# Kernel optimization log

Hardware: AMD Instinct MI355X
Metric: run time of the kernel (lower is better)

## Reference

```python
import jax, jax.numpy as jnp
import numpy as np

HEADS = 8
HEAD_DIM = 64
SCALE = HEAD_DIM ** -0.5


def setup_inputs() -> dict:
    key = jax.random.key(0)
    ks = jax.random.split(key, 5)
    d_model, inner = 1024, HEADS * HEAD_DIM  # 512
    x = jax.random.normal(ks[0], (2, 2048, d_model), dtype=jnp.float32)
    # torch Linear weights stored pre-transposed as [in, out]
    Wq = jax.random.normal(ks[1], (d_model, inner), dtype=jnp.float32) * (d_model ** -0.5)
    Wkv = jax.random.normal(ks[2], (d_model, 2 * inner), dtype=jnp.float32) * (d_model ** -0.5)
    Wo = jax.random.normal(ks[3], (inner, d_model), dtype=jnp.float32) * (inner ** -0.5)
    bo = jnp.zeros((d_model,), dtype=jnp.float32)
    return {"x": x, "Wq": Wq, "Wkv": Wkv, "Wo": Wo, "bo": bo}


def reference(x, Wq, Wkv, Wo, bo):
    b, n, _ = x.shape
    q = x @ Wq                       # [b, n, h*d]
    kv = x @ Wkv                     # [b, n, 2*h*d] (self-attention: context = x)
    k, v = jnp.split(kv, 2, axis=-1)

    def split_heads(t):
        return t.reshape(b, n, HEADS, HEAD_DIM).transpose(0, 2, 1, 3)  # [b, h, n, d]

    q, k, v = map(split_heads, (q, k, v))
    sim = jnp.einsum('bhid,bhjd->bhij', q, k) * SCALE  # [b, h, n, n]
    attn = jax.nn.softmax(sim, axis=-1)                # dropout p=0.0 -> identity
    out = jnp.einsum('bhij,bhjd->bhid', attn, v)       # [b, h, n, d]
    out = out.transpose(0, 2, 1, 3).reshape(b, n, HEADS * HEAD_DIM)
    return out @ Wo + bo
```

## Files before the change

kernel.cpp:

```cpp
#include <hip/hip_runtime.h>

typedef _Float16 f16;
typedef __attribute__((ext_vector_type(4))) _Float16 f16x4;
typedef __attribute__((ext_vector_type(8))) _Float16 f16x8;
typedef __attribute__((ext_vector_type(4))) float f32x4;

#define CEXP 0.18033688011112042f
#define QKB_LD 1056

__device__ __forceinline__ void gload16(const f16* g, f16* l) {
    __builtin_amdgcn_global_load_lds((const __attribute__((address_space(1))) void*)g,
                                     (__attribute__((address_space(3))) void*)l, 16, 0, 0);
}

__global__ __launch_bounds__(256) void conv_f32_f16_k(const float* __restrict__ in,
                                                      f16* __restrict__ out) {
    int idx = (blockIdx.x * 256 + threadIdx.x) * 8;
    float4 a = *(const float4*)(in + idx);
    float4 b = *(const float4*)(in + idx + 4);
    f16x8 o;
    o[0] = (f16)a.x; o[1] = (f16)a.y; o[2] = (f16)a.z; o[3] = (f16)a.w;
    o[4] = (f16)b.x; o[5] = (f16)b.y; o[6] = (f16)b.z; o[7] = (f16)b.w;
    *(f16x8*)(out + idx) = o;
}

__global__ __launch_bounds__(256) void transpose_conv_k(const float* __restrict__ in,
                                                        f16* __restrict__ out,
                                                        int N, int ldo, int row_off) {
    __shared__ float tile[32][33];
    int tx = threadIdx.x & 31, ty = threadIdx.x >> 5;
    int n0 = blockIdx.x * 32, k0 = blockIdx.y * 32;
#pragma unroll
    for (int j = 0; j < 4; j++)
        tile[ty + j * 8][tx] = in[(size_t)(k0 + ty + j * 8) * N + n0 + tx];
    __syncthreads();
#pragma unroll
    for (int j = 0; j < 4; j++)
        out[(size_t)(row_off + n0 + ty + j * 8) * ldo + k0 + tx] = (f16)tile[tx][ty + j * 8];
}

template <int MODE, int BN>
__global__ __launch_bounds__(256) void gemm_k(
    const f16* __restrict__ A, const f16* __restrict__ Bt,
    f16* __restrict__ Cqk, f16* __restrict__ Cvt,
    float* __restrict__ Cout, const float* __restrict__ bias,
    int K, int NTILES) {
    __shared__ __align__(16) f16 As[128 * 64];
    __shared__ __align__(16) f16 Bs[BN * 64];
    constexpr int MI = (BN == 128) ? 4 : 2;
    int bid = blockIdx.x;
    int nt = bid % NTILES, mt = bid / NTILES;
    int m0 = mt * 128, n0 = nt * BN;
    int tid = threadIdx.x;
    int lane = tid & 63, w = tid >> 6;
    int rowBase = (BN == 128) ? (w >> 1) * 64 : w * 32;
    int colBase = (BN == 128) ? (w & 1) * 64 : 0;
    int lr = lane & 15, lg = lane >> 4;
    int rowL = lane >> 3;
    int colL = (lane & 7) * 8;
    int bRow0 = (BN == 128) ? w * 32 : w * 16;
    const f16* aSrc = A + (size_t)(m0 + w * 32 + rowL) * K + colL;
    const f16* bSrc = Bt + (size_t)(n0 + bRow0 + rowL) * K + colL;
    f32x4 acc[MI][4] = {};

    for (int k0 = 0; k0 < K; k0 += 64) {
#pragma unroll
        for (int j = 0; j < 4; j++)
            gload16(aSrc + k0 + (size_t)(j * 8) * K, &As[(w * 32 + j * 8) * 64]);
#pragma unroll
        for (int j = 0; j < (BN == 128 ? 4 : 2); j++)
            gload16(bSrc + k0 + (size_t)(j * 8) * K, &Bs[(bRow0 + j * 8) * 64]);
        __syncthreads();
#pragma unroll
        for (int ks = 0; ks < 2; ks++) {
            f16x8 af[MI], bf[4];
#pragma unroll
            for (int i = 0; i < MI; i++)
                af[i] = *(const f16x8*)(&As[(rowBase + i * 16 + lr) * 64 + ks * 32 + lg * 8]);
#pragma unroll
            for (int j = 0; j < 4; j++)
                bf[j] = *(const f16x8*)(&Bs[(colBase + j * 16 + lr) * 64 + ks * 32 + lg * 8]);
#pragma unroll
            for (int i = 0; i < MI; i++)
#pragma unroll
                for (int j = 0; j < 4; j++)
                    acc[i][j] = __builtin_amdgcn_mfma_f32_16x16x32_f16(af[i], bf[j], acc[i][j], 0, 0, 0);
        }
        __syncthreads();
    }

#pragma unroll
    for (int i = 0; i < MI; i++) {
#pragma unroll
        for (int j = 0; j < 4; j++) {
            int row = m0 + rowBase + i * 16 + lg * 4;
            int col = n0 + colBase + j * 16 + lr;
            if (MODE == 1) {
                float bv = bias[col];
#pragma unroll
                for (int r = 0; r < 4; r++)
                    Cout[(size_t)(row + r) * 1024 + col] = acc[i][j][r] + bv;
            } else {
                if (col < 1024) {
                    float sc = (col < 512) ? CEXP : 1.0f;
#pragma unroll
                    for (int r = 0; r < 4; r++)
                        Cqk[(size_t)(row + r) * QKB_LD + col] = (f16)(acc[i][j][r] * sc);
                } else {
                    int c = col - 1024;
                    int hh = c >> 6, d = c & 63;
                    int bb = row >> 11, n = row & 2047;
                    int pr = bb * 8 + hh;
                    int tt = n >> 6, kvl = n & 63;
                    int kg = kvl >> 4, lga = (kvl >> 2) & 3;
                    int dgp = d >> 5, dh = (d >> 4) & 1, lra = d & 15;
                    f16x4 ov;
#pragma unroll
                    for (int r = 0; r < 4; r++) ov[r] = (f16)acc[i][j][r];
                    size_t idx = ((((size_t)(pr * 32 + tt) * 4 + kg) * 2 + dgp) * 64
                                  + lga * 16 + lra) * 8 + dh * 4;
                    *(f16x4*)(Cvt + idx) = ov;
                }
            }
        }
    }
}

__global__ __launch_bounds__(256, 2) void attn_k(const f16* __restrict__ qkb,
                                                 const f16* __restrict__ vt2,
                                                 f16* __restrict__ ao) {
    __shared__ __align__(16) f16 Ks[4 * 4096];
    __shared__ __align__(16) f16 Vs[3 * 4096];

    int bid = blockIdx.x;
    int xcd = bid & 7;
    int pair = xcd * 2 + ((bid >> 3) & 1);
    int qblk = bid >> 4;
    int b = pair >> 3, h = pair & 7;
    int tid = threadIdx.x;
    int lane = tid & 63, w = tid >> 6;
    int lr = lane & 15, lg = lane >> 4;
    int q0 = qblk * 64 + w * 16;

    const f16* qb = qkb + (size_t)b * 2048 * QKB_LD + h * 64;
    const f16* kb = qb + 512;

    f16x8 qf0 = *(const f16x8*)(qb + (size_t)(q0 + lr) * QKB_LD + lg * 8);
    f16x8 qf1 = *(const f16x8*)(qb + (size_t)(q0 + lr) * QKB_LD + 32 + lg * 8);
    asm volatile("s_waitcnt vmcnt(0)" ::: "memory");

    int srcCol = (((lane & 7) ^ (lane >> 3)) << 3);
    int rowL = lane >> 3;
    const f16* ksrc = kb + (size_t)(w * 16 + rowL) * QKB_LD + srcCol;
    const f16* vsrc = vt2 + ((size_t)(pair * 32) * 8 + 2 * w) * 512 + lane * 8;

    auto stageK = [&](int buf, int kv0) {
        f16* dst = &Ks[buf * 4096 + (w * 16) * 64];
        gload16(ksrc + (size_t)kv0 * QKB_LD, dst);
        gload16(ksrc + (size_t)(kv0 + 8) * QKB_LD, dst + 8 * 64);
    };
    auto stageV = [&](int buf, int tile) {
        const f16* s = vsrc + (size_t)tile * 4096;
        f16* dst = &Vs[buf * 4096 + (2 * w) * 512];
        gload16(s, dst);
        gload16(s + 512, dst + 512);
    };

    stageK(0, 0); stageV(0, 0); stageK(1, 64); stageV(1, 1); stageK(2, 128);
    asm volatile("s_waitcnt vmcnt(4)" ::: "memory");
    __builtin_amdgcn_s_barrier();
    asm volatile("" ::: "memory");

    int kOffA = (lg * 8) ^ ((lr & 7) << 3);

    f32x4 acc[4] = {};
    float m = -INFINITY, lp = 0.f;
    f32x4 sA[4], sB[4];

    {
        __builtin_amdgcn_s_setprio(1);
#pragma unroll
        for (int kg = 0; kg < 4; kg++) {
            const f16* krow = &Ks[(kg * 16 + lr) * 64];
            f16x8 ka0 = *(const f16x8*)(krow + kOffA);
            f16x8 ka1 = *(const f16x8*)(krow + (kOffA ^ 32));
            f32x4 z = {};
            z = __builtin_amdgcn_mfma_f32_16x16x32_f16(ka0, qf0, z, 0, 0, 0);
            sA[kg] = __builtin_amdgcn_mfma_f32_16x16x32_f16(ka1, qf1, z, 0, 0, 0);
        }
        __builtin_amdgcn_s_setprio(0);
    }

    auto body = [&](f32x4 (&sCur)[4], f32x4 (&sNxt)[4], int t, int vIdx) {
        if (t <= 28) stageK((t + 3) & 3, (t + 3) * 64);
        if (t <= 29) stageV(vIdx == 0 ? 2 : vIdx - 1, t + 2);

        if (t < 31) {
            const f16* kbuf = &Ks[((t + 1) & 3) * 4096];
            __builtin_amdgcn_s_setprio(1);
#pragma unroll
            for (int kg = 0; kg < 4; kg++) {
                const f16* krow = kbuf + (kg * 16 + lr) * 64;
                f16x8 ka0 = *(const f16x8*)(krow + kOffA);
                f16x8 ka1 = *(const f16x8*)(krow + (kOffA ^ 32));
                f32x4 z = {};
                z = __builtin_amdgcn_mfma_f32_16x16x32_f16(ka0, qf0, z, 0, 0, 0);
                sNxt[kg] = __builtin_amdgcn_mfma_f32_16x16x32_f16(ka1, qf1, z, 0, 0, 0);
            }
            __builtin_amdgcn_s_setprio(0);
        }

        float x0 = fmaxf(fmaxf(sCur[0][0], sCur[0][1]), fmaxf(sCur[0][2], sCur[0][3]));
        float x1 = fmaxf(fmaxf(sCur[1][0], sCur[1][1]), fmaxf(sCur[1][2], sCur[1][3]));
        float x2 = fmaxf(fmaxf(sCur[2][0], sCur[2][1]), fmaxf(sCur[2][2], sCur[2][3]));
        float x3 = fmaxf(fmaxf(sCur[3][0], sCur[3][1]), fmaxf(sCur[3][2], sCur[3][3]));
        float ownmx = fmaxf(fmaxf(x0, x1), fmaxf(x2, x3));
        if (!__all(ownmx - m <= 8.f)) {
            float mx = fmaxf(ownmx, __shfl_xor(ownmx, 16, 64));
            mx = fmaxf(mx, __shfl_xor(mx, 32, 64));
            float mn = fmaxf(m, mx);
            float alpha = __builtin_amdgcn_exp2f(m - mn);
            m = mn;
            lp *= alpha;
#pragma unroll
            for (int dg = 0; dg < 4; dg++)
#pragma unroll
                for (int r = 0; r < 4; r++) acc[dg][r] *= alpha;
        }
        f16x4 pf[4];
#pragma unroll
        for (int kg = 0; kg < 4; kg++) {
            float p0 = __builtin_amdgcn_exp2f(sCur[kg][0] - m);
            float p1 = __builtin_amdgcn_exp2f(sCur[kg][1] - m);
            float p2 = __builtin_amdgcn_exp2f(sCur[kg][2] - m);
            float p3 = __builtin_amdgcn_exp2f(sCur[kg][3] - m);
            pf[kg][0] = (f16)p0; pf[kg][1] = (f16)p1;
            pf[kg][2] = (f16)p2; pf[kg][3] = (f16)p3;
            lp += (p0 + p1) + (p2 + p3);
        }

        const f16* vl = &Vs[vIdx * 4096] + lane * 8;
        __builtin_amdgcn_s_setprio(1);
#pragma unroll
        for (int kg = 0; kg < 4; kg++)
#pragma unroll
            for (int dgp = 0; dgp < 2; dgp++) {
                f16x8 vv = *(const f16x8*)(vl + (kg * 2 + dgp) * 512);
                f16x4 vlo = __builtin_shufflevector(vv, vv, 0, 1, 2, 3);
                f16x4 vhi = __builtin_shufflevector(vv, vv, 4, 5, 6, 7);
                acc[dgp * 2]     = __builtin_amdgcn_mfma_f32_16x16x16f16(vlo, pf[kg], acc[dgp * 2], 0, 0, 0);
                acc[dgp * 2 + 1] = __builtin_amdgcn_mfma_f32_16x16x16f16(vhi, pf[kg], acc[dgp * 2 + 1], 0, 0, 0);
            }
        __builtin_amdgcn_s_setprio(0);

        if (t <= 28)      { asm volatile("s_waitcnt vmcnt(4)" ::: "memory"); }
        else if (t == 29) { asm volatile("s_waitcnt vmcnt(2)" ::: "memory"); }
        else if (t == 30) { asm volatile("s_waitcnt vmcnt(0)" ::: "memory"); }
        if (t < 31) {
            __builtin_amdgcn_s_barrier();
            asm volatile("" ::: "memory");
        }
    };

    int vIdx = 0;
    for (int u = 0; u < 16; u++) {
        body(sA, sB, 2 * u, vIdx);     vIdx = (vIdx == 2) ? 0 : vIdx + 1;
        body(sB, sA, 2 * u + 1, vIdx); vIdx = (vIdx == 2) ? 0 : vIdx + 1;
    }

    lp += __shfl_xor(lp, 16, 64);
    lp += __shfl_xor(lp, 32, 64);
    float inv = 1.f / lp;
#pragma unroll
    for (int dg = 0; dg < 4; dg++) {
        f16x4 ov;
#pragma unroll
        for (int r = 0; r < 4; r++) ov[r] = (f16)(acc[dg][r] * inv);
        *(f16x4*)(ao + (size_t)(b * 2048 + q0 + lr) * 512 + h * 64 + dg * 16 + lg * 4) = ov;
    }
}

extern "C" void kernel_launch(void* const* d_in, const int* in_sizes, int n_in,
                              void* d_out, int out_size, void* d_ws, size_t ws_size,
                              hipStream_t stream) {
    const float* x   = (const float*)d_in[0];
    const float* Wq  = (const float*)d_in[1];
    const float* Wkv = (const float*)d_in[2];
    const float* Wo  = (const float*)d_in[3];
    const float* bo  = (const float*)d_in[4];
    float* out = (float*)d_out;

    f16* xb    = (f16*)d_ws;
    f16* wqkvT = xb + 4096 * 1024;
    f16* woT   = wqkvT + 1536 * 1024;
    f16* qkb   = woT + 1024 * 512;
    f16* vtb2  = qkb + 4096 * QKB_LD;
    f16* ao    = vtb2 + 16 * 32 * 4096;

    conv_f32_f16_k<<<2048, 256, 0, stream>>>(x, xb);
    transpose_conv_k<<<dim3(16, 32), 256, 0, stream>>>(Wq, wqkvT, 512, 1024, 0);
    transpose_conv_k<<<dim3(32, 32), 256, 0, stream>>>(Wkv, wqkvT, 1024, 1024, 512);
    transpose_conv_k<<<dim3(32, 16), 256, 0, stream>>>(Wo, woT, 1024, 512, 0);

    gemm_k<0, 64><<<32 * 24, 256, 0, stream>>>(xb, wqkvT, qkb, vtb2, nullptr, nullptr, 1024, 24);
    attn_k<<<512, 256, 0, stream>>>(qkb, vtb2, ao);
    gemm_k<1, 128><<<32 * 8, 256, 0, stream>>>(ao, woT, nullptr, nullptr, out, bo, 512, 8);
}
```

Before: 93.51 us.

## Split attention KV range across waves and load K/V directly from global

Each block now handles 32 query rows, with two wave pairs each covering half of the KV sequence (split-K). Partial softmax states are merged through shared memory at the end. K and V fragments are loaded straight from global memory into registers, with K prefetched one tile ahead, replacing the LDS staging pipeline and its barriers. The grid doubles to 1024 blocks and occupancy rises to 3 blocks per CU. The trade-offs are lost K/V reuse through LDS across waves, more redundant global traffic, and exposed global-load latency.

```diff
diff --git a/kernel.cpp b/kernel.cpp
--- a/kernel.cpp
+++ b/kernel.cpp
@@ -126,11 +126,12 @@
     }
 }
 
-__global__ __launch_bounds__(256, 2) void attn_k(const f16* __restrict__ qkb,
+__global__ __launch_bounds__(256, 3) void attn_k(const f16* __restrict__ qkb,
                                                  const f16* __restrict__ vt2,
                                                  f16* __restrict__ ao) {
-    __shared__ __align__(16) f16 Ks[4 * 4096];
-    __shared__ __align__(16) f16 Vs[3 * 4096];
+    __shared__ float accS[4][64][16];
+    __shared__ float lpS[4][64];
+    __shared__ float mS[4][64];
 
     int bid = blockIdx.x;
     int xcd = bid & 7;
@@ -140,80 +141,59 @@
     int tid = threadIdx.x;
     int lane = tid & 63, w = tid >> 6;
     int lr = lane & 15, lg = lane >> 4;
-    int q0 = qblk * 64 + w * 16;
+    int qsub = w & 1, half = w >> 1;
+    int q0 = qblk * 32 + qsub * 16;
 
     const f16* qb = qkb + (size_t)b * 2048 * QKB_LD + h * 64;
     const f16* kb = qb + 512;
+    const f16* vbase = vt2 + ((size_t)pair * 32) * 4096 + lane * 8;
 
     f16x8 qf0 = *(const f16x8*)(qb + (size_t)(q0 + lr) * QKB_LD + lg * 8);
     f16x8 qf1 = *(const f16x8*)(qb + (size_t)(q0 + lr) * QKB_LD + 32 + lg * 8);
-    asm volatile("s_waitcnt vmcnt(0)" ::: "memory");
-
-    int srcCol = (((lane & 7) ^ (lane >> 3)) << 3);
-    int rowL = lane >> 3;
-    const f16* ksrc = kb + (size_t)(w * 16 + rowL) * QKB_LD + srcCol;
-    const f16* vsrc = vt2 + ((size_t)(pair * 32) * 8 + 2 * w) * 512 + lane * 8;
-
-    auto stageK = [&](int buf, int kv0) {
-        f16* dst = &Ks[buf * 4096 + (w * 16) * 64];
-        gload16(ksrc + (size_t)kv0 * QKB_LD, dst);
-        gload16(ksrc + (size_t)(kv0 + 8) * QKB_LD, dst + 8 * 64);
-    };
-    auto stageV = [&](int buf, int tile) {
-        const f16* s = vsrc + (size_t)tile * 4096;
-        f16* dst = &Vs[buf * 4096 + (2 * w) * 512];
-        gload16(s, dst);
-        gload16(s + 512, dst + 512);
-    };
-
-    stageK(0, 0); stageV(0, 0); stageK(1, 64); stageV(1, 1); stageK(2, 128);
-    asm volatile("s_waitcnt vmcnt(4)" ::: "memory");
-    __builtin_amdgcn_s_barrier();
-    asm volatile("" ::: "memory");
-
-    int kOffA = (lg * 8) ^ ((lr & 7) << 3);
+
+    const f16* krow = kb + (size_t)(half * 1024 + lr) * QKB_LD + lg * 8;
+
+    f16x8 ka0[4], ka1[4];
+#pragma unroll
+    for (int kg = 0; kg < 4; kg++) {
+        const f16* p = krow + (size_t)(kg * 16) * QKB_LD;
+        ka0[kg] = *(const f16x8*)(p);
+        ka1[kg] = *(const f16x8*)(p + 32);
+    }
 
     f32x4 acc[4] = {};
     float m = -INFINITY, lp = 0.f;
-    f32x4 sA[4], sB[4];
-
-    {
+
+    for (int t = 0; t < 16; t++) {
+        const f16* vl = vbase + (size_t)(half * 16 + t) * 4096;
+        f16x8 vv[8];
+#pragma unroll
+        for (int i = 0; i < 8; i++) vv[i] = *(const f16x8*)(vl + i * 512);
+
+        f32x4 s[4];
         __builtin_amdgcn_s_setprio(1);
 #pragma unroll
         for (int kg = 0; kg < 4; kg++) {
-            const f16* krow = &Ks[(kg * 16 + lr) * 64];
-            f16x8 ka0 = *(const f16x8*)(krow + kOffA);
-            f16x8 ka1 = *(const f16x8*)(krow + (kOffA ^ 32));
             f32x4 z = {};
-            z = __builtin_amdgcn_mfma_f32_16x16x32_f16(ka0, qf0, z, 0, 0, 0);
-            sA[kg] = __builtin_amdgcn_mfma_f32_16x16x32_f16(ka1, qf1, z, 0, 0, 0);
+            z = __builtin_amdgcn_mfma_f32_16x16x32_f16(ka0[kg], qf0, z, 0, 0, 0);
+            s[kg] = __builtin_amdgcn_mfma_f32_16x16x32_f16(ka1[kg], qf1, z, 0, 0, 0);
         }
         __builtin_amdgcn_s_setprio(0);
-    }
-
-    auto body = [&](f32x4 (&sCur)[4], f32x4 (&sNxt)[4], int t, int vIdx) {
-        if (t <= 28) stageK((t + 3) & 3, (t + 3) * 64);
-        if (t <= 29) stageV(vIdx == 0 ? 2 : vIdx - 1, t + 2);
-
-        if (t < 31) {
-            const f16* kbuf = &Ks[((t + 1) & 3) * 4096];
-            __builtin_amdgcn_s_setprio(1);
+
+        if (t < 15) {
+            const f16* p2 = krow + (size_t)((t + 1) * 64) * QKB_LD;
 #pragma unroll
             for (int kg = 0; kg < 4; kg++) {
-                const f16* krow = kbuf + (kg * 16 + lr) * 64;
-                f16x8 ka0 = *(const f16x8*)(krow + kOffA);
-                f16x8 ka1 = *(const f16x8*)(krow + (kOffA ^ 32));
-                f32x4 z = {};
-                z = __builtin_amdgcn_mfma_f32_16x16x32_f16(ka0, qf0, z, 0, 0, 0);
-                sNxt[kg] = __builtin_amdgcn_mfma_f32_16x16x32_f16(ka1, qf1, z, 0, 0, 0);
+                const f16* p = p2 + (size_t)(kg * 16) * QKB_LD;
+                ka0[kg] = *(const f16x8*)(p);
+                ka1[kg] = *(const f16x8*)(p + 32);
             }
-            __builtin_amdgcn_s_setprio(0);
-        }
-
-        float x0 = fmaxf(fmaxf(sCur[0][0], sCur[0][1]), fmaxf(sCur[0][2], sCur[0][3]));
-        float x1 = fmaxf(fmaxf(sCur[1][0], sCur[1][1]), fmaxf(sCur[1][2], sCur[1][3]));
-        float x2 = fmaxf(fmaxf(sCur[2][0], sCur[2][1]), fmaxf(sCur[2][2], sCur[2][3]));
-        float x3 = fmaxf(fmaxf(sCur[3][0], sCur[3][1]), fmaxf(sCur[3][2], sCur[3][3]));
+        }
+
+        float x0 = fmaxf(fmaxf(s[0][0], s[0][1]), fmaxf(s[0][2], s[0][3]));
+        float x1 = fmaxf(fmaxf(s[1][0], s[1][1]), fmaxf(s[1][2], s[1][3]));
+        float x2 = fmaxf(fmaxf(s[2][0], s[2][1]), fmaxf(s[2][2], s[2][3]));
+        float x3 = fmaxf(fmaxf(s[3][0], s[3][1]), fmaxf(s[3][2], s[3][3]));
         float ownmx = fmaxf(fmaxf(x0, x1), fmaxf(x2, x3));
         if (!__all(ownmx - m <= 8.f)) {
             float mx = fmaxf(ownmx, __shfl_xor(ownmx, 16, 64));
@@ -230,53 +210,53 @@
         f16x4 pf[4];
 #pragma unroll
         for (int kg = 0; kg < 4; kg++) {
-            float p0 = __builtin_amdgcn_exp2f(sCur[kg][0] - m);
-            float p1 = __builtin_amdgcn_exp2f(sCur[kg][1] - m);
-            float p2 = __builtin_amdgcn_exp2f(sCur[kg][2] - m);
-            float p3 = __builtin_amdgcn_exp2f(sCur[kg][3] - m);
+            float p0 = __builtin_amdgcn_exp2f(s[kg][0] - m);
+            float p1 = __builtin_amdgcn_exp2f(s[kg][1] - m);
+            float p2 = __builtin_amdgcn_exp2f(s[kg][2] - m);
+            float p3 = __builtin_amdgcn_exp2f(s[kg][3] - m);
             pf[kg][0] = (f16)p0; pf[kg][1] = (f16)p1;
             pf[kg][2] = (f16)p2; pf[kg][3] = (f16)p3;
             lp += (p0 + p1) + (p2 + p3);
         }
 
-        const f16* vl = &Vs[vIdx * 4096] + lane * 8;
         __builtin_amdgcn_s_setprio(1);
 #pragma unroll
         for (int kg = 0; kg < 4; kg++)
 #pragma unroll
             for (int dgp = 0; dgp < 2; dgp++) {
-                f16x8 vv = *(const f16x8*)(vl + (kg * 2 + dgp) * 512);
-                f16x4 vlo = __builtin_shufflevector(vv, vv, 0, 1, 2, 3);
-                f16x4 vhi = __builtin_shufflevector(vv, vv, 4, 5, 6, 7);
+                f16x8 vx = vv[kg * 2 + dgp];
+                f16x4 vlo = __builtin_shufflevector(vx, vx, 0, 1, 2, 3);
+                f16x4 vhi = __builtin_shufflevector(vx, vx, 4, 5, 6, 7);
                 acc[dgp * 2]     = __builtin_amdgcn_mfma_f32_16x16x16f16(vlo, pf[kg], acc[dgp * 2], 0, 0, 0);
                 acc[dgp * 2 + 1] = __builtin_amdgcn_mfma_f32_16x16x16f16(vhi, pf[kg], acc[dgp * 2 + 1], 0, 0, 0);
             }
         __builtin_amdgcn_s_setprio(0);
-
-        if (t <= 28)      { asm volatile("s_waitcnt vmcnt(4)" ::: "memory"); }
-        else if (t == 29) { asm volatile("s_waitcnt vmcnt(2)" ::: "memory"); }
-        else if (t == 30) { asm volatile("s_waitcnt vmcnt(0)" ::: "memory"); }
-        if (t < 31) {
-            __builtin_amdgcn_s_barrier();
-            asm volatile("" ::: "memory");
-        }
-    };
-
-    int vIdx = 0;
-    for (int u = 0; u < 16; u++) {
-        body(sA, sB, 2 * u, vIdx);     vIdx = (vIdx == 2) ? 0 : vIdx + 1;
-        body(sB, sA, 2 * u + 1, vIdx); vIdx = (vIdx == 2) ? 0 : vIdx + 1;
     }
 
     lp += __shfl_xor(lp, 16, 64);
     lp += __shfl_xor(lp, 32, 64);
-    float inv = 1.f / lp;
-#pragma unroll
-    for (int dg = 0; dg < 4; dg++) {
-        f16x4 ov;
-#pragma unroll
-        for (int r = 0; r < 4; r++) ov[r] = (f16)(acc[dg][r] * inv);
-        *(f16x4*)(ao + (size_t)(b * 2048 + q0 + lr) * 512 + h * 64 + dg * 16 + lg * 4) = ov;
+#pragma unroll
+    for (int dg = 0; dg < 4; dg++) *(f32x4*)&accS[w][lane][dg * 4] = acc[dg];
+    lpS[w][lane] = lp;
+    mS[w][lane] = m;
+    __syncthreads();
+
+    if (w < 2) {
+        float mP = mS[w + 2][lane];
+        float lpP = lpS[w + 2][lane];
+        float M = fmaxf(m, mP);
+        float a = __builtin_amdgcn_exp2f(m - M);
+        float c = __builtin_amdgcn_exp2f(mP - M);
+        float inv = 1.f / (lp * a + lpP * c);
+#pragma unroll
+        for (int dg = 0; dg < 4; dg++) {
+            f32x4 oP = *(const f32x4*)&accS[w + 2][lane][dg * 4];
+            f16x4 ov;
+#pragma unroll
+            for (int r = 0; r < 4; r++)
+                ov[r] = (f16)((acc[dg][r] * a + oP[r] * c) * inv);
+            *(f16x4*)(ao + (size_t)(b * 2048 + q0 + lr) * 512 + h * 64 + dg * 16 + lg * 4) = ov;
+        }
     }
 }
 
@@ -303,6 +283,6 @@
     transpose_conv_k<<<dim3(32, 16), 256, 0, stream>>>(Wo, woT, 1024, 512, 0);
 
     gemm_k<0, 64><<<32 * 24, 256, 0, stream>>>(xb, wqkvT, qkb, vtb2, nullptr, nullptr, 1024, 24);
-    attn_k<<<512, 256, 0, stream>>>(qkb, vtb2, ao);
+    attn_k<<<1024, 256, 0, stream>>>(qkb, vtb2, ao);
     gemm_k<1, 128><<<32 * 8, 256, 0, stream>>>(ao, woT, nullptr, nullptr, out, bo, 512, 8);
 }
```

New measurement: 110.7 us. 1.18x slower.

## Split attention KV range across two wave groups per block and merge partial softmax

Applied to the files above, without the earlier changes.

Each attention block now runs 512 threads: two halves of four waves each process half of the key/value sequence (16 tiles each) for the same query rows, with separate triple-buffered K and double-buffered V staging. At the end the second half writes its partial output, running sum and max to shared memory and the first half merges them with a log-sum-exp rescale. The aim is more waves per CU and a shorter serial KV loop per wave to hide latency, at the cost of the merge step, extra barriers, and a switch from fine-grained vmcnt waits to full __syncthreads.

```diff
diff --git a/kernel.cpp b/kernel.cpp
--- a/kernel.cpp
+++ b/kernel.cpp
@@ -126,11 +126,11 @@
     }
 }
 
-__global__ __launch_bounds__(256, 2) void attn_k(const f16* __restrict__ qkb,
+__global__ __launch_bounds__(512, 4) void attn_k(const f16* __restrict__ qkb,
                                                  const f16* __restrict__ vt2,
                                                  f16* __restrict__ ao) {
-    __shared__ __align__(16) f16 Ks[4 * 4096];
-    __shared__ __align__(16) f16 Vs[3 * 4096];
+    __shared__ __align__(16) f16 Ks[2][3 * 4096];
+    __shared__ __align__(16) f16 Vs[2][2 * 4096];
 
     int bid = blockIdx.x;
     int xcd = bid & 7;
@@ -139,37 +139,35 @@
     int b = pair >> 3, h = pair & 7;
     int tid = threadIdx.x;
     int lane = tid & 63, w = tid >> 6;
+    int half = w >> 2, wl = w & 3;
     int lr = lane & 15, lg = lane >> 4;
-    int q0 = qblk * 64 + w * 16;
+    int q0 = qblk * 64 + wl * 16;
 
     const f16* qb = qkb + (size_t)b * 2048 * QKB_LD + h * 64;
     const f16* kb = qb + 512;
 
     f16x8 qf0 = *(const f16x8*)(qb + (size_t)(q0 + lr) * QKB_LD + lg * 8);
     f16x8 qf1 = *(const f16x8*)(qb + (size_t)(q0 + lr) * QKB_LD + 32 + lg * 8);
-    asm volatile("s_waitcnt vmcnt(0)" ::: "memory");
 
     int srcCol = (((lane & 7) ^ (lane >> 3)) << 3);
     int rowL = lane >> 3;
-    const f16* ksrc = kb + (size_t)(w * 16 + rowL) * QKB_LD + srcCol;
-    const f16* vsrc = vt2 + ((size_t)(pair * 32) * 8 + 2 * w) * 512 + lane * 8;
-
-    auto stageK = [&](int buf, int kv0) {
-        f16* dst = &Ks[buf * 4096 + (w * 16) * 64];
-        gload16(ksrc + (size_t)kv0 * QKB_LD, dst);
-        gload16(ksrc + (size_t)(kv0 + 8) * QKB_LD, dst + 8 * 64);
+    const f16* ksrc = kb + (size_t)(half * 1024 + wl * 16 + rowL) * QKB_LD + srcCol;
+    const f16* vsrc = vt2 + ((size_t)(pair * 32 + half * 16) * 8 + 2 * wl) * 512 + lane * 8;
+
+    auto stageK = [&](int buf, int tt) {
+        f16* dst = &Ks[half][buf * 4096 + (wl * 16) * 64];
+        gload16(ksrc + (size_t)(tt * 64) * QKB_LD, dst);
+        gload16(ksrc + (size_t)(tt * 64 + 8) * QKB_LD, dst + 8 * 64);
     };
-    auto stageV = [&](int buf, int tile) {
-        const f16* s = vsrc + (size_t)tile * 4096;
-        f16* dst = &Vs[buf * 4096 + (2 * w) * 512];
+    auto stageV = [&](int buf, int tt) {
+        const f16* s = vsrc + (size_t)tt * 4096;
+        f16* dst = &Vs[half][buf * 4096 + (2 * wl) * 512];
         gload16(s, dst);
         gload16(s + 512, dst + 512);
     };
 
-    stageK(0, 0); stageV(0, 0); stageK(1, 64); stageV(1, 1); stageK(2, 128);
-    asm volatile("s_waitcnt vmcnt(4)" ::: "memory");
-    __builtin_amdgcn_s_barrier();
-    asm volatile("" ::: "memory");
+    stageK(0, 0); stageV(0, 0); stageK(1, 1);
+    __syncthreads();
 
     int kOffA = (lg * 8) ^ ((lr & 7) << 3);
 
@@ -181,7 +179,7 @@
         __builtin_amdgcn_s_setprio(1);
 #pragma unroll
         for (int kg = 0; kg < 4; kg++) {
-            const f16* krow = &Ks[(kg * 16 + lr) * 64];
+            const f16* krow = &Ks[half][(kg * 16 + lr) * 64];
             f16x8 ka0 = *(const f16x8*)(krow + kOffA);
             f16x8 ka1 = *(const f16x8*)(krow + (kOffA ^ 32));
             f32x4 z = {};
@@ -191,12 +189,12 @@
         __builtin_amdgcn_s_setprio(0);
     }
 
-    auto body = [&](f32x4 (&sCur)[4], f32x4 (&sNxt)[4], int t, int vIdx) {
-        if (t <= 28) stageK((t + 3) & 3, (t + 3) * 64);
-        if (t <= 29) stageV(vIdx == 0 ? 2 : vIdx - 1, t + 2);
-
-        if (t < 31) {
-            const f16* kbuf = &Ks[((t + 1) & 3) * 4096];
+    auto body = [&](f32x4 (&sCur)[4], f32x4 (&sNxt)[4], int t) {
+        if (t <= 13) stageK((t + 2) % 3, t + 2);
+        if (t <= 14) stageV((t + 1) & 1, t + 1);
+
+        if (t < 15) {
+            const f16* kbuf = &Ks[half][((t + 1) % 3) * 4096];
             __builtin_amdgcn_s_setprio(1);
 #pragma unroll
             for (int kg = 0; kg < 4; kg++) {
@@ -239,7 +237,7 @@
             lp += (p0 + p1) + (p2 + p3);
         }
 
-        const f16* vl = &Vs[vIdx * 4096] + lane * 8;
+        const f16* vl = &Vs[half][(t & 1) * 4096] + lane * 8;
         __builtin_amdgcn_s_setprio(1);
 #pragma unroll
         for (int kg = 0; kg < 4; kg++)
@@ -253,30 +251,44 @@
             }
         __builtin_amdgcn_s_setprio(0);
 
-        if (t <= 28)      { asm volatile("s_waitcnt vmcnt(4)" ::: "memory"); }
-        else if (t == 29) { asm volatile("s_waitcnt vmcnt(2)" ::: "memory"); }
-        else if (t == 30) { asm volatile("s_waitcnt vmcnt(0)" ::: "memory"); }
-        if (t < 31) {
-            __builtin_amdgcn_s_barrier();
-            asm volatile("" ::: "memory");
-        }
+        if (t < 15) __syncthreads();
     };
 
-    int vIdx = 0;
-    for (int u = 0; u < 16; u++) {
-        body(sA, sB, 2 * u, vIdx);     vIdx = (vIdx == 2) ? 0 : vIdx + 1;
-        body(sB, sA, 2 * u + 1, vIdx); vIdx = (vIdx == 2) ? 0 : vIdx + 1;
+    for (int u = 0; u < 8; u++) {
+        body(sA, sB, 2 * u);
+        body(sB, sA, 2 * u + 1);
     }
 
     lp += __shfl_xor(lp, 16, 64);
     lp += __shfl_xor(lp, 32, 64);
-    float inv = 1.f / lp;
-#pragma unroll
-    for (int dg = 0; dg < 4; dg++) {
-        f16x4 ov;
-#pragma unroll
-        for (int r = 0; r < 4; r++) ov[r] = (f16)(acc[dg][r] * inv);
-        *(f16x4*)(ao + (size_t)(b * 2048 + q0 + lr) * 512 + h * 64 + dg * 16 + lg * 4) = ov;
+    __syncthreads();
+    float* mO = (float*)&Ks[0][0];
+    float* mL = mO + 4 * 64 * 16;
+    float* mM = mL + 4 * 64;
+    if (half == 1) {
+#pragma unroll
+        for (int dg = 0; dg < 4; dg++)
+            *(f32x4*)&mO[(wl * 64 + lane) * 16 + dg * 4] = acc[dg];
+        mL[wl * 64 + lane] = lp;
+        mM[wl * 64 + lane] = m;
+    }
+    __syncthreads();
+    if (half == 0) {
+        float mP = mM[wl * 64 + lane];
+        float lpP = mL[wl * 64 + lane];
+        float M = fmaxf(m, mP);
+        float a = __builtin_amdgcn_exp2f(m - M);
+        float c = __builtin_amdgcn_exp2f(mP - M);
+        float inv = 1.f / (lp * a + lpP * c);
+#pragma unroll
+        for (int dg = 0; dg < 4; dg++) {
+            f32x4 oP = *(const f32x4*)&mO[(wl * 64 + lane) * 16 + dg * 4];
+            f16x4 ov;
+#pragma unroll
+            for (int r = 0; r < 4; r++)
+                ov[r] = (f16)((acc[dg][r] * a + oP[r] * c) * inv);
+            *(f16x4*)(ao + (size_t)(b * 2048 + q0 + lr) * 512 + h * 64 + dg * 16 + lg * 4) = ov;
+        }
     }
 }
 
@@ -303,6 +315,6 @@
     transpose_conv_k<<<dim3(32, 16), 256, 0, stream>>>(Wo, woT, 1024, 512, 0);
 
     gemm_k<0, 64><<<32 * 24, 256, 0, stream>>>(xb, wqkvT, qkb, vtb2, nullptr, nullptr, 1024, 24);
-    attn_k<<<512, 256, 0, stream>>>(qkb, vtb2, ao);
+    attn_k<<<512, 512, 0, stream>>>(qkb, vtb2, ao);
     gemm_k<1, 128><<<32 * 8, 256, 0, stream>>>(ao, woT, nullptr, nullptr, out, bo, 512, 8);
 }
```

New measurement: 90.08 us. 3.7% less time.
